# Performance work log

Hardware: AMD Instinct MI355X
Metric: run time of the kernel (lower is better)

## Reference

```python
import jax, jax.numpy as jnp
import numpy as np

B, S, D, F, E, K = 4, 1024, 512, 1024, 8, 2
LB_W, Z_W = 0.01, 0.001

def setup_inputs() -> dict:
    key = jax.random.key(0)
    k1, k2, k3, k4, k5 = jax.random.split(key, 5)
    std = 0.02
    x = jax.random.normal(k1, (B, S, D), dtype=jnp.float32)
    router_w = jax.random.normal(k2, (E, D), dtype=jnp.float32) * std  # nn.Linear weight [out,in]
    gate_w = jax.random.normal(k3, (E, D, F), dtype=jnp.float32) * std
    up_w = jax.random.normal(k4, (E, D, F), dtype=jnp.float32) * std
    down_w = jax.random.normal(k5, (E, F, D), dtype=jnp.float32) * std
    return {"x": x, "router_w": router_w, "gate_w": gate_w, "up_w": up_w, "down_w": down_w}

def reference(x, router_w, gate_w, up_w, down_w):
    b, s, d = x.shape
    e = router_w.shape[0]
    xf = x.reshape(-1, d)                      # [T, D]
    T = xf.shape[0]
    logits = xf @ router_w.T                   # [T, E]
    probs = jax.nn.softmax(logits, axis=-1)
    top_v, top_i = jax.lax.top_k(probs, K)     # [T, K]
    top_v = top_v / jnp.sum(top_v, axis=-1, keepdims=True)
    # combine[t, e] = sum_k top_v[t,k] * [top_i[t,k] == e]  (matches index_add_ accumulation)
    combine = jnp.zeros((T, e), dtype=xf.dtype).at[jnp.arange(T)[:, None], top_i].add(top_v)
    # SwiGLU experts, dense over E with weighted combine (same math as gather/scatter path)
    h_gate = jnp.einsum('td,edf->etf', xf, gate_w)   # [E, T, F]
    h_up = jnp.einsum('td,edf->etf', xf, up_w)       # [E, T, F]
    hidden = jax.nn.silu(h_gate) * h_up
    out = jnp.einsum('etf,efd,te->td', hidden, down_w, combine)  # [T, D]
    # auxiliary losses
    expert_mask = jax.nn.one_hot(top_i, e, dtype=jnp.float32).sum(axis=1)  # [T, E]
    f = expert_mask.sum(axis=0) / (T * K)
    P = probs.mean(axis=0)
    load_balance_loss = e * jnp.sum(f * P)
    z_loss = jnp.mean(jnp.square(jax.scipy.special.logsumexp(logits, axis=-1)))
    aux_loss = LB_W * load_balance_loss + Z_W * z_loss
    return out.reshape(b, s, d), aux_loss
```

## Files before the change

kernel.cpp:

```cpp
#include <hip/hip_runtime.h>

#define T_TOK 4096
#define D_DIM 512
#define F_DIM 1024
#define E_NUM 8
#define CAP   2048
#define BM    128
#define BN    64
#define BK    64
#define MT    (CAP/BM)
#define NT_GU (F_DIM/BN)
#define NT_DN (D_DIM/BN)
#define RB_TOK 32
#define CSTRIDE 32

typedef __bf16 bf16x8 __attribute__((ext_vector_type(8)));
typedef float  f32x4  __attribute__((ext_vector_type(4)));

__device__ __forceinline__ unsigned short f2bf(float f){
  unsigned int u = __builtin_bit_cast(unsigned int, f);
  u += 0x7FFFu + ((u >> 16) & 1u);
  return (unsigned short)(u >> 16);
}

__device__ __forceinline__ void gload16(const void* g, void* l){
  __builtin_amdgcn_global_load_lds(
      (const __attribute__((address_space(1))) unsigned int*)g,
      (__attribute__((address_space(3))) unsigned int*)l, 16, 0, 0);
}

__global__ __launch_bounds__(256) void transpose_kernel(
    const float* __restrict__ in, unsigned short* __restrict__ outb, int R, int C){
  int e = blockIdx.z;
  int c0 = blockIdx.x*64, r0 = blockIdx.y*64;
  const float* src = in + (size_t)e*R*C;
  unsigned short* dst = outb + (size_t)e*R*C;
  __shared__ unsigned short tile[64][66];
  int tid = threadIdx.x;
  #pragma unroll
  for (int i=0;i<16;i++){
    int idx = i*256+tid; int rl = idx>>6, cl = idx&63;
    tile[cl][rl] = f2bf(src[(size_t)(r0+rl)*C + (c0+cl)]);
  }
  __syncthreads();
  #pragma unroll
  for (int i=0;i<16;i++){
    int idx = i*256+tid; int cl = idx>>6, rl = idx&63;
    dst[(size_t)(c0+cl)*R + (r0+rl)] = tile[cl][rl];
  }
}

__global__ __launch_bounds__(256) void router_kernel(
    const float* __restrict__ x, const float* __restrict__ rw,
    unsigned short* __restrict__ Xg,
    int* __restrict__ cnt, int* __restrict__ slot_token, float* __restrict__ slot_w,
    float* __restrict__ Psum, float* __restrict__ zsum){
  __shared__ float rws[E_NUM*D_DIM];
  __shared__ float lp[RB_TOK][E_NUM];
  __shared__ float lw1[RB_TOK], lw2[RB_TOK], llse[RB_TOK];
  __shared__ int   li1[RB_TOK], li2[RB_TOK];
  __shared__ int   lsl1[RB_TOK], lsl2[RB_TOK];
  int tid = threadIdx.x, wid = tid>>6, lane = tid&63;
  for (int i = tid; i < E_NUM*D_DIM; i += 256) rws[i] = rw[i];
  __syncthreads();

  uint4 pk[8];
  #pragma unroll
  for (int i=0;i<8;i++){
    int widx = wid*8 + i;
    int t = blockIdx.x*RB_TOK + widx;
    const float* xr = x + (size_t)t*D_DIM + lane*8;
    float4 xa = *(const float4*)xr;
    float4 xc = *(const float4*)(xr+4);
    pk[i].x = (unsigned)f2bf(xa.x) | ((unsigned)f2bf(xa.y)<<16);
    pk[i].y = (unsigned)f2bf(xa.z) | ((unsigned)f2bf(xa.w)<<16);
    pk[i].z = (unsigned)f2bf(xc.x) | ((unsigned)f2bf(xc.y)<<16);
    pk[i].w = (unsigned)f2bf(xc.z) | ((unsigned)f2bf(xc.w)<<16);

    float logit[E_NUM];
    #pragma unroll
    for (int e=0;e<E_NUM;e++){
      const float* wr = rws + e*D_DIM + lane*8;
      float4 wa = *(const float4*)wr;
      float4 wb = *(const float4*)(wr+4);
      float s = xa.x*wa.x + xa.y*wa.y + xa.z*wa.z + xa.w*wa.w
              + xc.x*wb.x + xc.y*wb.y + xc.z*wb.z + xc.w*wb.w;
      #pragma unroll
      for (int m=1;m<64;m<<=1) s += __shfl_xor(s, m);
      logit[e] = s;
    }
    float mx = logit[0];
    #pragma unroll
    for (int e=1;e<E_NUM;e++) mx = fmaxf(mx, logit[e]);
    float p[E_NUM]; float s = 0.f;
    #pragma unroll
    for (int e=0;e<E_NUM;e++){ p[e] = __expf(logit[e]-mx); s += p[e]; }
    float inv = 1.f/s;
    #pragma unroll
    for (int e=0;e<E_NUM;e++) p[e] *= inv;
    float lse = mx + __logf(s);
    int i1 = 0;
    #pragma unroll
    for (int e=1;e<E_NUM;e++) if (logit[e] > logit[i1]) i1 = e;
    int i2 = (i1==0) ? 1 : 0;
    #pragma unroll
    for (int e=0;e<E_NUM;e++) if (e != i1 && logit[e] > logit[i2]) i2 = e;
    if (lane == 0){
      float v1 = p[i1], v2 = p[i2];
      float invw = 1.f/(v1+v2);
      li1[widx] = i1; li2[widx] = i2;
      lw1[widx] = v1*invw; lw2[widx] = v2*invw;
      llse[widx] = lse;
      #pragma unroll
      for (int e=0;e<E_NUM;e++) lp[widx][e] = p[e];
    }
  }
  __syncthreads();

  if (tid < E_NUM){
    int e = tid, c = 0;
    #pragma unroll 4
    for (int j=0;j<RB_TOK;j++) c += (li1[j]==e) + (li2[j]==e);
    int idx = atomicAdd(&cnt[e*CSTRIDE], c);
    int tbase = blockIdx.x*RB_TOK;
    for (int j=0;j<RB_TOK;j++){
      if (li1[j]==e){ slot_token[e*CAP+idx] = tbase+j; slot_w[e*CAP+idx] = lw1[j]; lsl1[j] = e*CAP+idx; idx++; }
      if (li2[j]==e){ slot_token[e*CAP+idx] = tbase+j; slot_w[e*CAP+idx] = lw2[j]; lsl2[j] = e*CAP+idx; idx++; }
    }
    float ps = 0.f;
    #pragma unroll 4
    for (int j=0;j<RB_TOK;j++) ps += lp[j][e];
    atomicAdd(&Psum[e*CSTRIDE], ps);
  } else if (tid == 64){
    float zs = 0.f;
    #pragma unroll 4
    for (int j=0;j<RB_TOK;j++){ float l = llse[j]; zs += l*l; }
    atomicAdd(zsum, zs);
  }
  __syncthreads();

  #pragma unroll
  for (int i=0;i<8;i++){
    int widx = wid*8 + i;
    int s1 = lsl1[widx], s2 = lsl2[widx];
    *(uint4*)((char*)Xg + (size_t)s1*(D_DIM*2) + lane*16) = pk[i];
    *(uint4*)((char*)Xg + (size_t)s2*(D_DIM*2) + lane*16) = pk[i];
  }
}

__global__ void finalize_kernel(const int* __restrict__ cnt, const float* __restrict__ Psum,
                                const float* __restrict__ zsum, int* __restrict__ off,
                                float* __restrict__ aux){
  if (threadIdx.x == 0 && blockIdx.x == 0){
    int o = 0; float lb = 0.f;
    #pragma unroll
    for (int e=0;e<E_NUM;e++){
      off[e] = o; o += cnt[e*CSTRIDE];
      float f = (float)cnt[e*CSTRIDE] / (float)(T_TOK*2);
      float P = Psum[e*CSTRIDE] / (float)T_TOK;
      lb += f*P;
    }
    float z = zsum[0] / (float)T_TOK;
    aux[0] = 0.01f * ((float)E_NUM * lb) + 0.001f * z;
  }
}

__global__ __launch_bounds__(256) void gemm_gateup(
    const unsigned short* __restrict__ Xg, const unsigned short* __restrict__ gwt,
    const unsigned short* __restrict__ uwt,
    const int* __restrict__ cnt, const int* __restrict__ off,
    const float* __restrict__ slot_w, unsigned short* __restrict__ H)
{
  int fid = blockIdx.x;
  int nid = (fid & 7)*(E_NUM*MT*NT_GU/8) + (fid >> 3);
  int e  = nid >> 8;
  int r  = nid & 255;
  int n0 = (r >> 4) * BN;
  int mt = r & 15;
  int c = cnt[e*CSTRIDE];
  int row0 = mt*BM;
  if (row0 >= c) return;
  int rem = c - row0;
  int tid = threadIdx.x, wid = tid>>6, lane = tid&63;
  __shared__ unsigned short lds[BM*BK + 2*BN*BK];
  unsigned short* As = lds;
  unsigned short* Bg = lds + BM*BK;
  unsigned short* Bu = Bg + BN*BK;

  int sub = lane>>3;
  int skb = ((lane&7)<<4) ^ (sub<<4);
  const char* asrc[4];
  #pragma unroll
  for (int i=0;i<4;i++){
    int rr = (wid*4+i)*8 + sub;
    asrc[i] = (const char*)Xg + ((size_t)e*CAP + row0 + rr)*(D_DIM*2) + skb;
  }
  const char* bgsrc[2]; const char* busrc[2];
  #pragma unroll
  for (int i=0;i<2;i++){
    int rr = (wid*2+i)*8 + sub;
    size_t rowb = ((size_t)e*F_DIM + n0 + rr) * (D_DIM*2);
    bgsrc[i] = (const char*)gwt + rowb + skb;
    busrc[i] = (const char*)uwt + rowb + skb;
  }

  f32x4 accg[4][2] = {};
  f32x4 accu[4][2] = {};
  int wm = wid>>1, wn = wid&1;

  size_t koff = 0;
  for (int kt=0; kt<D_DIM/BK; ++kt, koff += BK*2){
    #pragma unroll
    for (int i=0;i<4;i++)
      gload16(asrc[i]+koff, (char*)As + (wid*4+i)*1024);
    #pragma unroll
    for (int i=0;i<2;i++){
      gload16(bgsrc[i]+koff, (char*)Bg + (wid*2+i)*1024);
      gload16(busrc[i]+koff, (char*)Bu + (wid*2+i)*1024);
    }
    __syncthreads();
    #pragma unroll
    for (int s=0;s<2;s++){
      int kc = s*4 + (lane>>4);
      bf16x8 a[4], bg[2], bu[2];
      #pragma unroll
      for (int m=0;m<4;m++){
        int ar = wm*64 + m*16 + (lane&15);
        a[m] = *(const bf16x8*)((const char*)As + ar*128 + ((kc<<4) ^ ((ar&7)<<4)));
      }
      #pragma unroll
      for (int n=0;n<2;n++){
        int br = wn*32 + n*16 + (lane&15);
        int bo = br*128 + ((kc<<4) ^ ((br&7)<<4));
        bg[n] = *(const bf16x8*)((const char*)Bg + bo);
        bu[n] = *(const bf16x8*)((const char*)Bu + bo);
      }
      #pragma unroll
      for (int m=0;m<4;m++){
        #pragma unroll
        for (int n=0;n<2;n++){
          accg[m][n] = __builtin_amdgcn_mfma_f32_16x16x32_bf16(a[m], bg[n], accg[m][n], 0,0,0);
          accu[m][n] = __builtin_amdgcn_mfma_f32_16x16x32_bf16(a[m], bu[n], accu[m][n], 0,0,0);
        }
      }
    }
    __syncthreads();
  }

  int offe = off[e];
  #pragma unroll
  for (int m=0;m<4;m++){
    #pragma unroll
    for (int j=0;j<4;j++){
      int row = wm*64 + m*16 + ((lane>>4)<<2) + j;
      if (row < rem){
        float wgt = slot_w[e*CAP + row0 + row];
        size_t hb = (size_t)(offe + row0 + row)*F_DIM;
        #pragma unroll
        for (int n=0;n<2;n++){
          int col = n0 + wn*32 + n*16 + (lane&15);
          float g = accg[m][n][j];
          float u = accu[m][n][j];
          float h = g * (1.f/(1.f+__expf(-g))) * u * wgt;
          H[hb + col] = f2bf(h);
        }
      }
    }
  }
}

__global__ __launch_bounds__(256) void gemm_down(
    const unsigned short* __restrict__ H, const unsigned short* __restrict__ dwt,
    const int* __restrict__ cnt, const int* __restrict__ off,
    const int* __restrict__ slot_token, float* __restrict__ out)
{
  int fid = blockIdx.x;
  int nid = (fid & 7)*(E_NUM*MT*NT_DN/8) + (fid >> 3);
  int e  = nid >> 7;
  int r  = nid & 127;
  int n0 = (r >> 4) * BN;
  int mt = r & 15;
  int c = cnt[e*CSTRIDE];
  int row0 = mt*BM;
  if (row0 >= c) return;
  int rem = c - row0;
  int tid = threadIdx.x, wid = tid>>6, lane = tid&63;
  __shared__ unsigned short lds[BM*BK + BN*BK];
  unsigned short* As = lds;
  unsigned short* Bs = lds + BM*BK;
  int sub = lane>>3;
  int skb = ((lane&7)<<4) ^ (sub<<4);
  int offe = off[e];
  const char* asrc[4];
  #pragma unroll
  for (int i=0;i<4;i++){
    int rr = (wid*4+i)*8 + sub;
    asrc[i] = (const char*)H + ((size_t)offe + row0 + rr)*(F_DIM*2) + skb;
  }
  const char* bsrc[2];
  #pragma unroll
  for (int i=0;i<2;i++){
    int rr = (wid*2+i)*8 + sub;
    bsrc[i] = (const char*)dwt + ((size_t)e*D_DIM + n0 + rr)*(F_DIM*2) + skb;
  }
  f32x4 acc[4][2] = {};
  int wm = wid>>1, wn = wid&1;
  size_t koff = 0;
  for (int kt=0; kt<F_DIM/BK; ++kt, koff += BK*2){
    #pragma unroll
    for (int i=0;i<4;i++) gload16(asrc[i]+koff, (char*)As + (wid*4+i)*1024);
    #pragma unroll
    for (int i=0;i<2;i++) gload16(bsrc[i]+koff, (char*)Bs + (wid*2+i)*1024);
    __syncthreads();
    #pragma unroll
    for (int s=0;s<2;s++){
      int kc = s*4 + (lane>>4);
      bf16x8 a[4], b[2];
      #pragma unroll
      for (int m=0;m<4;m++){
        int ar = wm*64 + m*16 + (lane&15);
        a[m] = *(const bf16x8*)((const char*)As + ar*128 + ((kc<<4) ^ ((ar&7)<<4)));
      }
      #pragma unroll
      for (int n=0;n<2;n++){
        int br = wn*32 + n*16 + (lane&15);
        b[n] = *(const bf16x8*)((const char*)Bs + br*128 + ((kc<<4) ^ ((br&7)<<4)));
      }
      #pragma unroll
      for (int m=0;m<4;m++){
        #pragma unroll
        for (int n=0;n<2;n++)
          acc[m][n] = __builtin_amdgcn_mfma_f32_16x16x32_bf16(a[m], b[n], acc[m][n], 0,0,0);
      }
    }
    __syncthreads();
  }
  #pragma unroll
  for (int m=0;m<4;m++){
    #pragma unroll
    for (int j=0;j<4;j++){
      int row = wm*64 + m*16 + ((lane>>4)<<2) + j;
      if (row < rem){
        int tok = slot_token[e*CAP + row0 + row];
        #pragma unroll
        for (int n=0;n<2;n++){
          int col = n0 + wn*32 + n*16 + (lane&15);
          atomicAdd(&out[(size_t)tok*D_DIM + col], acc[m][n][j]);
        }
      }
    }
  }
}

extern "C" void kernel_launch(void* const* d_in, const int* in_sizes, int n_in,
                              void* d_out, int out_size, void* d_ws, size_t ws_size,
                              hipStream_t stream){
  const float* x  = (const float*)d_in[0];
  const float* rw = (const float*)d_in[1];
  const float* gw = (const float*)d_in[2];
  const float* uw = (const float*)d_in[3];
  const float* dw = (const float*)d_in[4];
  float* out = (float*)d_out;

  char* w = (char*)d_ws;
  unsigned short* Xg  = (unsigned short*)w;  w += (size_t)E_NUM*CAP*D_DIM*2;
  unsigned short* gwt = (unsigned short*)w;  w += (size_t)E_NUM*D_DIM*F_DIM*2;
  unsigned short* uwt = (unsigned short*)w;  w += (size_t)E_NUM*D_DIM*F_DIM*2;
  unsigned short* dwt = (unsigned short*)w;  w += (size_t)E_NUM*F_DIM*D_DIM*2;
  unsigned short* H   = (unsigned short*)w;  w += (size_t)(T_TOK*2 + BM)*F_DIM*2;
  int*   slot_token = (int*)w;               w += (size_t)E_NUM*CAP*4;
  float* slot_w     = (float*)w;             w += (size_t)E_NUM*CAP*4;
  char* meta = w;
  int*   cnt  = (int*)w;       w += E_NUM*CSTRIDE*4;
  int*   off  = (int*)w;       w += 128;
  float* Psum = (float*)w;     w += E_NUM*CSTRIDE*4;
  float* zsum = (float*)w;     w += 128;
  size_t meta_bytes = (size_t)(w - meta);

  hipMemsetAsync(d_out, 0, (size_t)out_size*sizeof(float), stream);
  hipMemsetAsync(meta, 0, meta_bytes, stream);

  transpose_kernel<<<dim3(F_DIM/64, D_DIM/64, E_NUM), 256, 0, stream>>>(gw, gwt, D_DIM, F_DIM);
  transpose_kernel<<<dim3(F_DIM/64, D_DIM/64, E_NUM), 256, 0, stream>>>(uw, uwt, D_DIM, F_DIM);
  transpose_kernel<<<dim3(D_DIM/64, F_DIM/64, E_NUM), 256, 0, stream>>>(dw, dwt, F_DIM, D_DIM);
  router_kernel<<<T_TOK/RB_TOK, 256, 0, stream>>>(x, rw, Xg, cnt, slot_token, slot_w, Psum, zsum);
  finalize_kernel<<<1, 64, 0, stream>>>(cnt, Psum, zsum, off, out + (size_t)T_TOK*D_DIM);
  gemm_gateup<<<E_NUM*MT*NT_GU, 256, 0, stream>>>(Xg, gwt, uwt, cnt, off, slot_w, H);
  gemm_down<<<E_NUM*MT*NT_DN, 256, 0, stream>>>(H, dwt, cnt, off, slot_token, out);
}
```

Baseline: 221.4 us.

## Merge transposes and router into one prep kernel; double-buffer GEMM LDS tiles

After: 197.0 us. 11.0% less time.

```diff
diff --git a/kernel.cpp b/kernel.cpp
--- a/kernel.cpp
+++ b/kernel.cpp
@@ -13,6 +13,10 @@
 #define NT_DN (D_DIM/BN)
 #define RB_TOK 32
 #define CSTRIDE 32
+#define RTR_BLOCKS (T_TOK/RB_TOK)
+
+#define GU_HALF (BM*BK*2 + 2*BN*BK*2)
+#define DN_HALF (BM*BK*2 + BN*BK*2)
 
 typedef __bf16 bf16x8 __attribute__((ext_vector_type(8)));
 typedef float  f32x4  __attribute__((ext_vector_type(4)));
@@ -29,38 +33,57 @@
       (__attribute__((address_space(3))) unsigned int*)l, 16, 0, 0);
 }
 
-__global__ __launch_bounds__(256) void transpose_kernel(
-    const float* __restrict__ in, unsigned short* __restrict__ outb, int R, int C){
-  int e = blockIdx.z;
-  int c0 = blockIdx.x*64, r0 = blockIdx.y*64;
-  const float* src = in + (size_t)e*R*C;
-  unsigned short* dst = outb + (size_t)e*R*C;
-  __shared__ unsigned short tile[64][66];
+__global__ __launch_bounds__(256) void prep_kernel(
+    const float* __restrict__ x, const float* __restrict__ rw,
+    const float* __restrict__ gw, const float* __restrict__ uw, const float* __restrict__ dw,
+    unsigned short* __restrict__ Xg,
+    unsigned short* __restrict__ gwt, unsigned short* __restrict__ uwt, unsigned short* __restrict__ dwt,
+    int* __restrict__ cnt, int* __restrict__ slot_token, float* __restrict__ slot_w,
+    float* __restrict__ Psum, float* __restrict__ zsum)
+{
+  __shared__ __align__(16) char smem[18432];
+  int b = blockIdx.x;
   int tid = threadIdx.x;
-  #pragma unroll
-  for (int i=0;i<16;i++){
-    int idx = i*256+tid; int rl = idx>>6, cl = idx&63;
-    tile[cl][rl] = f2bf(src[(size_t)(r0+rl)*C + (c0+cl)]);
-  }
-  __syncthreads();
-  #pragma unroll
-  for (int i=0;i<16;i++){
-    int idx = i*256+tid; int cl = idx>>6, rl = idx&63;
-    dst[(size_t)(c0+cl)*R + (r0+rl)] = tile[cl][rl];
-  }
-}
-
-__global__ __launch_bounds__(256) void router_kernel(
-    const float* __restrict__ x, const float* __restrict__ rw,
-    unsigned short* __restrict__ Xg,
-    int* __restrict__ cnt, int* __restrict__ slot_token, float* __restrict__ slot_w,
-    float* __restrict__ Psum, float* __restrict__ zsum){
-  __shared__ float rws[E_NUM*D_DIM];
-  __shared__ float lp[RB_TOK][E_NUM];
-  __shared__ float lw1[RB_TOK], lw2[RB_TOK], llse[RB_TOK];
-  __shared__ int   li1[RB_TOK], li2[RB_TOK];
-  __shared__ int   lsl1[RB_TOK], lsl2[RB_TOK];
-  int tid = threadIdx.x, wid = tid>>6, lane = tid&63;
+
+  if (b >= RTR_BLOCKS){
+    int tb = b - RTR_BLOCKS;
+    int seg = tb >> 10;
+    int r1023 = tb & 1023;
+    int e = r1023 >> 7;
+    int rr = r1023 & 127;
+    const float* in; unsigned short* outp; int R, C, nbx;
+    if (seg == 0){ in = gw; outp = gwt; R = D_DIM; C = F_DIM; nbx = F_DIM/64; }
+    else if (seg == 1){ in = uw; outp = uwt; R = D_DIM; C = F_DIM; nbx = F_DIM/64; }
+    else { in = dw; outp = dwt; R = F_DIM; C = D_DIM; nbx = D_DIM/64; }
+    int c0 = (rr % nbx)*64, r0 = (rr / nbx)*64;
+    const float* src = in + (size_t)e*R*C;
+    unsigned short* dst = outp + (size_t)e*R*C;
+    unsigned short (*tile)[66] = (unsigned short(*)[66])smem;
+    #pragma unroll
+    for (int i=0;i<16;i++){
+      int idx = i*256+tid; int rl = idx>>6, cl = idx&63;
+      tile[cl][rl] = f2bf(src[(size_t)(r0+rl)*C + (c0+cl)]);
+    }
+    __syncthreads();
+    #pragma unroll
+    for (int i=0;i<16;i++){
+      int idx = i*256+tid; int cl = idx>>6, rl = idx&63;
+      dst[(size_t)(c0+cl)*R + (r0+rl)] = tile[cl][rl];
+    }
+    return;
+  }
+
+  float* rws          = (float*)smem;
+  float (*lp)[E_NUM]  = (float(*)[E_NUM])(smem+16384);
+  float* lw1          = (float*)(smem+17408);
+  float* lw2          = (float*)(smem+17536);
+  float* llse         = (float*)(smem+17664);
+  int*   li1          = (int*)(smem+17792);
+  int*   li2          = (int*)(smem+17920);
+  int*   lsl1         = (int*)(smem+18048);
+  int*   lsl2         = (int*)(smem+18176);
+
+  int wid = tid>>6, lane = tid&63;
   for (int i = tid; i < E_NUM*D_DIM; i += 256) rws[i] = rw[i];
   __syncthreads();
 
@@ -68,7 +91,7 @@
   #pragma unroll
   for (int i=0;i<8;i++){
     int widx = wid*8 + i;
-    int t = blockIdx.x*RB_TOK + widx;
+    int t = b*RB_TOK + widx;
     const float* xr = x + (size_t)t*D_DIM + lane*8;
     float4 xa = *(const float4*)xr;
     float4 xc = *(const float4*)(xr+4);
@@ -122,7 +145,7 @@
     #pragma unroll 4
     for (int j=0;j<RB_TOK;j++) c += (li1[j]==e) + (li2[j]==e);
     int idx = atomicAdd(&cnt[e*CSTRIDE], c);
-    int tbase = blockIdx.x*RB_TOK;
+    int tbase = b*RB_TOK;
     for (int j=0;j<RB_TOK;j++){
       if (li1[j]==e){ slot_token[e*CAP+idx] = tbase+j; slot_w[e*CAP+idx] = lw1[j]; lsl1[j] = e*CAP+idx; idx++; }
       if (li2[j]==e){ slot_token[e*CAP+idx] = tbase+j; slot_w[e*CAP+idx] = lw2[j]; lsl2[j] = e*CAP+idx; idx++; }
@@ -182,10 +205,7 @@
   if (row0 >= c) return;
   int rem = c - row0;
   int tid = threadIdx.x, wid = tid>>6, lane = tid&63;
-  __shared__ unsigned short lds[BM*BK + 2*BN*BK];
-  unsigned short* As = lds;
-  unsigned short* Bg = lds + BM*BK;
-  unsigned short* Bu = Bg + BN*BK;
+  __shared__ __align__(16) char arena[2*GU_HALF];
 
   int sub = lane>>3;
   int skb = ((lane&7)<<4) ^ (sub<<4);
@@ -208,17 +228,23 @@
   f32x4 accu[4][2] = {};
   int wm = wid>>1, wn = wid&1;
 
-  size_t koff = 0;
-  for (int kt=0; kt<D_DIM/BK; ++kt, koff += BK*2){
+  auto STAGE = [&](int buf, int kt){
+    size_t ko = (size_t)kt*BK*2;
+    char* base = arena + buf*GU_HALF;
     #pragma unroll
     for (int i=0;i<4;i++)
-      gload16(asrc[i]+koff, (char*)As + (wid*4+i)*1024);
+      gload16(asrc[i]+ko, base + (wid*4+i)*1024);
     #pragma unroll
     for (int i=0;i<2;i++){
-      gload16(bgsrc[i]+koff, (char*)Bg + (wid*2+i)*1024);
-      gload16(busrc[i]+koff, (char*)Bu + (wid*2+i)*1024);
-    }
-    __syncthreads();
+      gload16(bgsrc[i]+ko, base + BM*BK*2 + (wid*2+i)*1024);
+      gload16(busrc[i]+ko, base + BM*BK*2 + BN*BK*2 + (wid*2+i)*1024);
+    }
+  };
+  auto COMPUTE = [&](int buf){
+    const char* base = arena + buf*GU_HALF;
+    const char* As = base;
+    const char* Bg = base + BM*BK*2;
+    const char* Bu = base + BM*BK*2 + BN*BK*2;
     #pragma unroll
     for (int s=0;s<2;s++){
       int kc = s*4 + (lane>>4);
@@ -226,14 +252,14 @@
       #pragma unroll
       for (int m=0;m<4;m++){
         int ar = wm*64 + m*16 + (lane&15);
-        a[m] = *(const bf16x8*)((const char*)As + ar*128 + ((kc<<4) ^ ((ar&7)<<4)));
+        a[m] = *(const bf16x8*)(As + ar*128 + ((kc<<4) ^ ((ar&7)<<4)));
       }
       #pragma unroll
       for (int n=0;n<2;n++){
         int br = wn*32 + n*16 + (lane&15);
         int bo = br*128 + ((kc<<4) ^ ((br&7)<<4));
-        bg[n] = *(const bf16x8*)((const char*)Bg + bo);
-        bu[n] = *(const bf16x8*)((const char*)Bu + bo);
+        bg[n] = *(const bf16x8*)(Bg + bo);
+        bu[n] = *(const bf16x8*)(Bu + bo);
       }
       #pragma unroll
       for (int m=0;m<4;m++){
@@ -244,8 +270,18 @@
         }
       }
     }
+  };
+
+  STAGE(0, 0);
+  __syncthreads();
+  int cur = 0;
+  for (int kt=0; kt<D_DIM/BK-1; ++kt){
+    STAGE(cur^1, kt+1);
+    COMPUTE(cur);
     __syncthreads();
-  }
+    cur ^= 1;
+  }
+  COMPUTE(cur);
 
   int offe = off[e];
   #pragma unroll
@@ -285,9 +321,7 @@
   if (row0 >= c) return;
   int rem = c - row0;
   int tid = threadIdx.x, wid = tid>>6, lane = tid&63;
-  __shared__ unsigned short lds[BM*BK + BN*BK];
-  unsigned short* As = lds;
-  unsigned short* Bs = lds + BM*BK;
+  __shared__ __align__(16) char arena[2*DN_HALF];
   int sub = lane>>3;
   int skb = ((lane&7)<<4) ^ (sub<<4);
   int offe = off[e];
@@ -305,36 +339,53 @@
   }
   f32x4 acc[4][2] = {};
   int wm = wid>>1, wn = wid&1;
-  size_t koff = 0;
-  for (int kt=0; kt<F_DIM/BK; ++kt, koff += BK*2){
-    #pragma unroll
-    for (int i=0;i<4;i++) gload16(asrc[i]+koff, (char*)As + (wid*4+i)*1024);
-    #pragma unroll
-    for (int i=0;i<2;i++) gload16(bsrc[i]+koff, (char*)Bs + (wid*2+i)*1024);
-    __syncthreads();
+
+  auto STAGE = [&](int buf, int kt){
+    size_t ko = (size_t)kt*BK*2;
+    char* base = arena + buf*DN_HALF;
+    #pragma unroll
+    for (int i=0;i<4;i++) gload16(asrc[i]+ko, base + (wid*4+i)*1024);
+    #pragma unroll
+    for (int i=0;i<2;i++) gload16(bsrc[i]+ko, base + BM*BK*2 + (wid*2+i)*1024);
+  };
+  auto COMPUTE = [&](int buf){
+    const char* base = arena + buf*DN_HALF;
+    const char* As = base;
+    const char* Bs = base + BM*BK*2;
     #pragma unroll
     for (int s=0;s<2;s++){
       int kc = s*4 + (lane>>4);
-      bf16x8 a[4], b[2];
+      bf16x8 a[4], bb[2];
       #pragma unroll
       for (int m=0;m<4;m++){
         int ar = wm*64 + m*16 + (lane&15);
-        a[m] = *(const bf16x8*)((const char*)As + ar*128 + ((kc<<4) ^ ((ar&7)<<4)));
+        a[m] = *(const bf16x8*)(As + ar*128 + ((kc<<4) ^ ((ar&7)<<4)));
       }
       #pragma unroll
       for (int n=0;n<2;n++){
         int br = wn*32 + n*16 + (lane&15);
-        b[n] = *(const bf16x8*)((const char*)Bs + br*128 + ((kc<<4) ^ ((br&7)<<4)));
+        bb[n] = *(const bf16x8*)(Bs + br*128 + ((kc<<4) ^ ((br&7)<<4)));
       }
       #pragma unroll
       for (int m=0;m<4;m++){
         #pragma unroll
         for (int n=0;n<2;n++)
-          acc[m][n] = __builtin_amdgcn_mfma_f32_16x16x32_bf16(a[m], b[n], acc[m][n], 0,0,0);
-      }
-    }
+          acc[m][n] = __builtin_amdgcn_mfma_f32_16x16x32_bf16(a[m], bb[n], acc[m][n], 0,0,0);
+      }
+    }
+  };
+
+  STAGE(0, 0);
+  __syncthreads();
+  int cur = 0;
+  for (int kt=0; kt<F_DIM/BK-1; ++kt){
+    STAGE(cur^1, kt+1);
+    COMPUTE(cur);
     __syncthreads();
-  }
+    cur ^= 1;
+  }
+  COMPUTE(cur);
+
   #pragma unroll
   for (int m=0;m<4;m++){
     #pragma unroll
@@ -377,13 +428,11 @@
   float* zsum = (float*)w;     w += 128;
   size_t meta_bytes = (size_t)(w - meta);
 
-  hipMemsetAsync(d_out, 0, (size_t)out_size*sizeof(float), stream);
-  hipMemsetAsync(meta, 0, meta_bytes, stream);
-
-  transpose_kernel<<<dim3(F_DIM/64, D_DIM/64, E_NUM), 256, 0, stream>>>(gw, gwt, D_DIM, F_DIM);
-  transpose_kernel<<<dim3(F_DIM/64, D_DIM/64, E_NUM), 256, 0, stream>>>(uw, uwt, D_DIM, F_DIM);
-  transpose_kernel<<<dim3(D_DIM/64, F_DIM/64, E_NUM), 256, 0, stream>>>(dw, dwt, F_DIM, D_DIM);
-  router_kernel<<<T_TOK/RB_TOK, 256, 0, stream>>>(x, rw, Xg, cnt, slot_token, slot_w, Psum, zsum);
+  (void)hipMemsetAsync(d_out, 0, (size_t)out_size*sizeof(float), stream);
+  (void)hipMemsetAsync(meta, 0, meta_bytes, stream);
+
+  prep_kernel<<<RTR_BLOCKS + 3*1024, 256, 0, stream>>>(
+      x, rw, gw, uw, dw, Xg, gwt, uwt, dwt, cnt, slot_token, slot_w, Psum, zsum);
   finalize_kernel<<<1, 64, 0, stream>>>(cnt, Psum, zsum, off, out + (size_t)T_TOK*D_DIM);
   gemm_gateup<<<E_NUM*MT*NT_GU, 256, 0, stream>>>(Xg, gwt, uwt, cnt, off, slot_w, H);
   gemm_down<<<E_NUM*MT*NT_DN, 256, 0, stream>>>(H, dwt, cnt, off, slot_token, out);
```
